# Kernel optimization log

Measured on AMD Instinct MI355X. Metric: run time of the kernel, lower is better.

## Reference

```python
import jax, jax.numpy as jnp
import numpy as np

B, S, D = 8, 4096, 64
LN_EPS = 1e-3  # keras LayerNormalization default epsilon


def setup_inputs() -> dict:
    key = jax.random.key(0)
    k1, k2 = jax.random.split(key)
    x = jax.random.normal(k1, (B, S, D), dtype=jnp.float32)
    # (D,D,D) concept tensor, scaled small like glorot-ish init
    concept_map = jax.random.normal(k2, (D, D, D), dtype=jnp.float32) * 0.02
    gamma = jnp.ones((D,), dtype=jnp.float32)
    beta = jnp.zeros((D,), dtype=jnp.float32)
    return {"x": x, "concept_map": concept_map, "gamma": gamma, "beta": beta}


def reference(x, concept_map, gamma, beta):
    b, s, d = x.shape
    # Causal Toeplitz decay matrix: T[i, j] = 1/(i-j)^2 for j < i, else 0.
    idx = jnp.arange(s)
    diff = idx[:, None] - idx[None, :]  # (S, S)
    T = jnp.where(diff > 0, 1.0 / (jnp.maximum(diff, 1).astype(x.dtype) ** 2), 0.0)
    # Weighted causal prefix sum: S_pre[b, i, c] = sum_{j<i} x[b, j, c] / (i-j)^2
    s_pre = jnp.einsum('ij,bjc->bic', T, x)
    # Bilinear form with concept tensor: out[b,i,k] = sum_{a,c} x[b,i,a] * s_pre[b,i,c] * W[k,a,c]
    outer = (x[:, :, :, None] * s_pre[:, :, None, :]).reshape(b, s, d * d)  # (B,S,D*D)
    out = outer @ concept_map.reshape(d, d * d).T  # (B,S,D)
    # Residual + LayerNorm (axis=-1, keras defaults). Dropout is identity at inference.
    r = out + x
    mu = jnp.mean(r, axis=-1, keepdims=True)
    var = jnp.mean((r - mu) ** 2, axis=-1, keepdims=True)
    y = (r - mu) / jnp.sqrt(var + LN_EPS) * gamma + beta
    return y
```

## Files before the change

### kernel.cpp

```cpp
#include <hip/hip_runtime.h>

#define S_DIM 4096
#define B_DIM 8
#define D_DIM 64
#define LN_EPS 1e-3f

typedef _Float16 half8 __attribute__((ext_vector_type(8)));
typedef float f32x4 __attribute__((ext_vector_type(4)));

__device__ __forceinline__ void async_copy16(void* lds, const void* gsrc) {
    __builtin_amdgcn_global_load_lds(
        (const __attribute__((address_space(1))) unsigned int*)gsrc,
        (__attribute__((address_space(3))) unsigned int*)lds, 16, 0, 0);
}

__global__ __launch_bounds__(256) void prep_stage1(const float* __restrict__ x,
                                                   const float* __restrict__ W,
                                                   _Float16* __restrict__ wt,
                                                   _Float16* __restrict__ s_out) {
    if (blockIdx.x < 1024) {
        int idx = blockIdx.x * 256 + threadIdx.x;
        int a = idx >> 12;
        int k = (idx >> 6) & 63;
        int c = idx & 63;
        wt[idx] = (_Float16)W[((k << 6) + a) * 64 + c];
        return;
    }
    const int lin = blockIdx.x - 1024;
    const int it = lin & 63;
    const int by = lin >> 6;
    const int i0 = it * 64;
    const int tid = threadIdx.x;
    const int w = tid >> 6, l = tid & 63, lg = l >> 4, lr = l & 15;

    __shared__ _Float16 Bs[64 * 72];

    f32x4 acc[4] = {};
    const float iRowF = (float)(i0 + w * 16 + lr);
    const int ldC = tid & 63;
    const int ldJ = (tid >> 6) * 16;

    const int jt0 = (it >= 2) ? (it - 2) : 0;
    for (int jt = jt0; jt <= it; ++jt) {
        const int j0 = jt * 64;
        __syncthreads();
        {
            const float* xp = x + ((size_t)by * S_DIM + j0 + ldJ) * D_DIM + ldC;
            half8 v0, v1;
            #pragma unroll
            for (int q = 0; q < 8; ++q) {
                v0[q] = (_Float16)xp[q * D_DIM];
                v1[q] = (_Float16)xp[(8 + q) * D_DIM];
            }
            *(half8*)&Bs[ldC * 72 + ldJ] = v0;
            *(half8*)&Bs[ldC * 72 + ldJ + 8] = v1;
        }
        __syncthreads();
        #pragma unroll
        for (int kk = 0; kk < 2; ++kk) {
            half8 af;
            #pragma unroll
            for (int bq = 0; bq < 8; ++bq) {
                int j = j0 + kk * 32 + lg * 8 + bq;
                float df = iRowF - (float)j;
                float tv = (df > 0.f) ? __builtin_amdgcn_rcpf(df * df) : 0.f;
                af[bq] = (_Float16)tv;
            }
            #pragma unroll
            for (int nt = 0; nt < 4; ++nt) {
                half8 bf = *(const half8*)&Bs[(nt * 16 + lr) * 72 + kk * 32 + lg * 8];
                acc[nt] = __builtin_amdgcn_mfma_f32_16x16x32_f16(af, bf, acc[nt], 0, 0, 0);
            }
        }
    }

    #pragma unroll
    for (int nt = 0; nt < 4; ++nt) {
        #pragma unroll
        for (int r = 0; r < 4; ++r) {
            int i = i0 + w * 16 + lg * 4 + r;
            int c = nt * 16 + lr;
            s_out[((size_t)by * S_DIM + i) * D_DIM + c] = (_Float16)acc[nt][r];
        }
    }
}

__global__ __launch_bounds__(512, 2) void stage2(const float* __restrict__ x,
                                                 const _Float16* __restrict__ s,
                                                 const _Float16* __restrict__ wt,
                                                 const float* __restrict__ gamma,
                                                 const float* __restrict__ beta,
                                                 float* __restrict__ out) {
    const int r0 = blockIdx.x * 128;
    const int tid = threadIdx.x;
    const int w = tid >> 6, l = tid & 63, lg = l >> 4, lr = l & 15;
    const int rg = w & 1;
    const int ah = w >> 1;

    __shared__ __align__(16) char smem[101376];
    _Float16* Xf = (_Float16*)smem;
    char* WbB = smem + 18432;
    float* P = (float*)smem;

    const int laneSrc = ((l >> 3) * 128) + ((((l & 7) ^ (l >> 3)) << 4));
    const char* wbase = (const char*)wt;

#define STAGE(t, buf)                                                          \
    {                                                                          \
        _Pragma("unroll")                                                      \
        for (int i_ = 0; i_ < 4; ++i_) {                                       \
            int c_ = w * 4 + i_;                                               \
            int q_ = c_ >> 3, sub_ = c_ & 7;                                   \
            const char* g_ = wbase + (size_t)(q_ * 16 + (t)) * 8192            \
                             + sub_ * 1024 + laneSrc;                          \
            char* l_ = WbB + (buf) * 32768 + q_ * 8192 + sub_ * 1024;          \
            async_copy16(l_, g_);                                              \
        }                                                                      \
    }

    STAGE(0, 0);
    STAGE(1, 1);

    {
        #pragma unroll
        for (int h = 0; h < 2; ++h) {
            int idx = h * 512 + tid;
            int row = idx >> 3, c0 = (idx & 7) * 8;
            const float* xp = x + (size_t)(r0 + row) * 64 + c0;
            half8 v;
            #pragma unroll
            for (int j = 0; j < 8; ++j) v[j] = (_Float16)xp[j];
            *(half8*)&Xf[row * 72 + c0] = v;
        }
    }

    half8 sf[4][2];
    #pragma unroll
    for (int rt = 0; rt < 4; ++rt) {
        size_t row = (size_t)(r0 + rg * 64 + rt * 16 + lr) * 64;
        sf[rt][0] = *(const half8*)&s[row + lg * 8];
        sf[rt][1] = *(const half8*)&s[row + 32 + lg * 8];
    }

    __syncthreads();

    half8 xav[4][2];
    #pragma unroll
    for (int rt = 0; rt < 4; ++rt)
        #pragma unroll
        for (int q = 0; q < 2; ++q)
            xav[rt][q] = *(const half8*)&Xf[(rg * 64 + rt * 16 + lr) * 72 + ah * 16 + q * 8];

    f32x4 acc[4][4] = {};
    const int swz0 = (lg * 16) ^ ((lr & 7) << 4);
    const int swz1 = (64 + lg * 16) ^ ((lr & 7) << 4);

    #pragma unroll
    for (int t = 0; t < 16; ++t) {
        const char* wa = WbB + (t & 1) * 32768 + ah * 8192;
        half8 af[4][2];
        #pragma unroll
        for (int rt = 0; rt < 4; ++rt) {
            _Float16 xa = xav[rt][t >> 3][t & 7];
            af[rt][0] = sf[rt][0] * xa;
            af[rt][1] = sf[rt][1] * xa;
        }
        #pragma unroll
        for (int nt = 0; nt < 4; ++nt) {
            const char* rp = wa + (nt * 16 + lr) * 128;
            half8 b0 = *(const half8*)(rp + swz0);
            half8 b1 = *(const half8*)(rp + swz1);
            #pragma unroll
            for (int rt = 0; rt < 4; ++rt) {
                acc[rt][nt] = __builtin_amdgcn_mfma_f32_16x16x32_f16(af[rt][0], b0, acc[rt][nt], 0, 0, 0);
                acc[rt][nt] = __builtin_amdgcn_mfma_f32_16x16x32_f16(af[rt][1], b1, acc[rt][nt], 0, 0, 0);
            }
        }
        __builtin_amdgcn_s_barrier();
        if (t + 2 < 16) STAGE(t + 2, t & 1);
        if (t < 14) {
            asm volatile("s_waitcnt vmcnt(4)" ::: "memory");
            __builtin_amdgcn_s_barrier();
        } else if (t == 14) {
            asm volatile("s_waitcnt vmcnt(0)" ::: "memory");
            __builtin_amdgcn_s_barrier();
        }
    }

    if (ah != 0) {
        const int ph = ah - 1;
        #pragma unroll
        for (int rt = 0; rt < 4; ++rt)
            #pragma unroll
            for (int nt = 0; nt < 4; ++nt)
                #pragma unroll
                for (int reg = 0; reg < 4; ++reg) {
                    int row_l = rg * 64 + rt * 16 + lg * 4 + reg;
                    P[ph * 8448 + row_l * 66 + nt * 16 + lr] = acc[rt][nt][reg];
                }
    }
    __syncthreads();

    if (ah == 0) {
        float gba[4], bta[4];
        #pragma unroll
        for (int nt = 0; nt < 4; ++nt) {
            gba[nt] = gamma[nt * 16 + lr];
            bta[nt] = beta[nt * 16 + lr];
        }
        #pragma unroll
        for (int rt = 0; rt < 4; ++rt) {
            float rv[4][4], sum[4], ssq[4];
            #pragma unroll
            for (int reg = 0; reg < 4; ++reg) {
                int row_l = rg * 64 + rt * 16 + lg * 4 + reg;
                size_t gr = (size_t)(r0 + row_l);
                float s_ = 0.f, q_ = 0.f;
                #pragma unroll
                for (int nt = 0; nt < 4; ++nt) {
                    int col = nt * 16 + lr;
                    float v = acc[rt][nt][reg]
                            + P[row_l * 66 + col]
                            + P[8448 + row_l * 66 + col]
                            + P[16896 + row_l * 66 + col]
                            + x[gr * 64 + col];
                    rv[nt][reg] = v;
                    s_ += v;
                    q_ += v * v;
                }
                sum[reg] = s_;
                ssq[reg] = q_;
            }
            #pragma unroll
            for (int m = 1; m < 16; m <<= 1) {
                #pragma unroll
                for (int reg = 0; reg < 4; ++reg) {
                    sum[reg] += __shfl_xor(sum[reg], m, 64);
                    ssq[reg] += __shfl_xor(ssq[reg], m, 64);
                }
            }
            #pragma unroll
            for (int reg = 0; reg < 4; ++reg) {
                float mean = sum[reg] * (1.f / 64.f);
                float var = ssq[reg] * (1.f / 64.f) - mean * mean;
                float rstd = __frsqrt_rn(var + LN_EPS);
                int gr = r0 + rg * 64 + rt * 16 + lg * 4 + reg;
                #pragma unroll
                for (int nt = 0; nt < 4; ++nt) {
                    float y = (rv[nt][reg] - mean) * rstd * gba[nt] + bta[nt];
                    out[(size_t)gr * 64 + nt * 16 + lr] = y;
                }
            }
        }
    }
#undef STAGE
}

extern "C" void kernel_launch(void* const* d_in, const int* in_sizes, int n_in,
                              void* d_out, int out_size, void* d_ws, size_t ws_size,
                              hipStream_t stream) {
    const float* x     = (const float*)d_in[0];
    const float* W     = (const float*)d_in[1];
    const float* gamma = (const float*)d_in[2];
    const float* beta  = (const float*)d_in[3];
    float* outp        = (float*)d_out;

    char* ws = (char*)d_ws;
    _Float16* s_f16 = (_Float16*)ws;
    _Float16* wt    = (_Float16*)(ws + (size_t)B_DIM * S_DIM * D_DIM * 2);

    prep_stage1<<<1024 + 512, 256, 0, stream>>>(x, W, wt, s_f16);
    stage2<<<(B_DIM * S_DIM) / 128, 512, 0, stream>>>(x, s_f16, wt, gamma, beta, outp);
}
```

Before: 33.71 us.

## Give each wave a private W slice to drop block barriers in stage2

Stage2 now uses 256-thread blocks over 64 rows. Each of the 4 waves owns a private 16 KB LDS double buffer and streams its own quarter of the `a` dimension of W, so the per-step block-wide s_barriers go away and waves synchronise only on their own vmcnt. The x tile is loaded straight from global memory into registers per wave instead of through shared LDS. All four waves now contribute partial sums to the LayerNorm epilogue through LDS. In exchange, each row block re-reads the full W per wave with no sharing, there are twice as many blocks, and total W traffic doubles.

```diff
diff --git a/kernel.cpp b/kernel.cpp
--- a/kernel.cpp
+++ b/kernel.cpp
@@ -85,71 +85,57 @@
     }
 }
 
-__global__ __launch_bounds__(512, 2) void stage2(const float* __restrict__ x,
+__global__ __launch_bounds__(256, 2) void stage2(const float* __restrict__ x,
                                                  const _Float16* __restrict__ s,
                                                  const _Float16* __restrict__ wt,
                                                  const float* __restrict__ gamma,
                                                  const float* __restrict__ beta,
                                                  float* __restrict__ out) {
-    const int r0 = blockIdx.x * 128;
+    const int r0 = blockIdx.x * 64;
     const int tid = threadIdx.x;
     const int w = tid >> 6, l = tid & 63, lg = l >> 4, lr = l & 15;
-    const int rg = w & 1;
-    const int ah = w >> 1;
-
-    __shared__ __align__(16) char smem[101376];
-    _Float16* Xf = (_Float16*)smem;
-    char* WbB = smem + 18432;
-    float* P = (float*)smem;
+
+    __shared__ __align__(16) char smem[65536];
+    char* myBuf = smem + w * 16384;
 
     const int laneSrc = ((l >> 3) * 128) + ((((l & 7) ^ (l >> 3)) << 4));
-    const char* wbase = (const char*)wt;
-
-#define STAGE(t, buf)                                                          \
+    const char* wbase = (const char*)wt + (size_t)w * 16 * 8192;
+
+#define STAGEW(t_, buf_)                                                       \
     {                                                                          \
         _Pragma("unroll")                                                      \
-        for (int i_ = 0; i_ < 4; ++i_) {                                       \
-            int c_ = w * 4 + i_;                                               \
-            int q_ = c_ >> 3, sub_ = c_ & 7;                                   \
-            const char* g_ = wbase + (size_t)(q_ * 16 + (t)) * 8192            \
-                             + sub_ * 1024 + laneSrc;                          \
-            char* l_ = WbB + (buf) * 32768 + q_ * 8192 + sub_ * 1024;          \
-            async_copy16(l_, g_);                                              \
-        }                                                                      \
-    }
-
-    STAGE(0, 0);
-    STAGE(1, 1);
-
-    {
-        #pragma unroll
-        for (int h = 0; h < 2; ++h) {
-            int idx = h * 512 + tid;
-            int row = idx >> 3, c0 = (idx & 7) * 8;
-            const float* xp = x + (size_t)(r0 + row) * 64 + c0;
-            half8 v;
-            #pragma unroll
-            for (int j = 0; j < 8; ++j) v[j] = (_Float16)xp[j];
-            *(half8*)&Xf[row * 72 + c0] = v;
-        }
+        for (int s_ = 0; s_ < 8; ++s_)                                         \
+            async_copy16(myBuf + (buf_) * 8192 + s_ * 1024,                    \
+                         wbase + (size_t)(t_) * 8192 + s_ * 1024 + laneSrc);   \
     }
 
     half8 sf[4][2];
     #pragma unroll
     for (int rt = 0; rt < 4; ++rt) {
-        size_t row = (size_t)(r0 + rg * 64 + rt * 16 + lr) * 64;
+        size_t row = (size_t)(r0 + rt * 16 + lr) * 64;
         sf[rt][0] = *(const half8*)&s[row + lg * 8];
         sf[rt][1] = *(const half8*)&s[row + 32 + lg * 8];
     }
-
-    __syncthreads();
-
     half8 xav[4][2];
     #pragma unroll
-    for (int rt = 0; rt < 4; ++rt)
-        #pragma unroll
-        for (int q = 0; q < 2; ++q)
-            xav[rt][q] = *(const half8*)&Xf[(rg * 64 + rt * 16 + lr) * 72 + ah * 16 + q * 8];
+    for (int rt = 0; rt < 4; ++rt) {
+        const float* xp = x + (size_t)(r0 + rt * 16 + lr) * 64 + w * 16;
+        half8 h0, h1;
+        #pragma unroll
+        for (int j = 0; j < 8; ++j) {
+            h0[j] = (_Float16)xp[j];
+            h1[j] = (_Float16)xp[8 + j];
+        }
+        xav[rt][0] = h0;
+        xav[rt][1] = h1;
+    }
+
+    __builtin_amdgcn_sched_barrier(0);
+    STAGEW(0, 0);
+    STAGEW(1, 1);
+    __builtin_amdgcn_sched_barrier(0);
+    asm volatile("s_waitcnt vmcnt(0)" ::: "memory");
+    __builtin_amdgcn_sched_barrier(0);
 
     f32x4 acc[4][4] = {};
     const int swz0 = (lg * 16) ^ ((lr & 7) << 4);
@@ -157,7 +143,7 @@
 
     #pragma unroll
     for (int t = 0; t < 16; ++t) {
-        const char* wa = WbB + (t & 1) * 32768 + ah * 8192;
+        const char* wa = myBuf + (t & 1) * 8192;
         half8 af[4][2];
         #pragma unroll
         for (int rt = 0; rt < 4; ++rt) {
@@ -176,84 +162,78 @@
                 acc[rt][nt] = __builtin_amdgcn_mfma_f32_16x16x32_f16(af[rt][1], b1, acc[rt][nt], 0, 0, 0);
             }
         }
-        __builtin_amdgcn_s_barrier();
-        if (t + 2 < 16) STAGE(t + 2, t & 1);
-        if (t < 14) {
-            asm volatile("s_waitcnt vmcnt(4)" ::: "memory");
-            __builtin_amdgcn_s_barrier();
+        if (t + 2 < 16) {
+            __builtin_amdgcn_sched_barrier(0);
+            STAGEW(t + 2, t & 1);
+            asm volatile("s_waitcnt vmcnt(8)" ::: "memory");
+            __builtin_amdgcn_sched_barrier(0);
         } else if (t == 14) {
             asm volatile("s_waitcnt vmcnt(0)" ::: "memory");
-            __builtin_amdgcn_s_barrier();
-        }
-    }
-
-    if (ah != 0) {
-        const int ph = ah - 1;
-        #pragma unroll
-        for (int rt = 0; rt < 4; ++rt)
-            #pragma unroll
-            for (int nt = 0; nt < 4; ++nt)
-                #pragma unroll
-                for (int reg = 0; reg < 4; ++reg) {
-                    int row_l = rg * 64 + rt * 16 + lg * 4 + reg;
-                    P[ph * 8448 + row_l * 66 + nt * 16 + lr] = acc[rt][nt][reg];
-                }
-    }
+            __builtin_amdgcn_sched_barrier(0);
+        }
+    }
+
+    float* Pw = (float*)myBuf;
+    #pragma unroll
+    for (int rt = 0; rt < 4; ++rt)
+        #pragma unroll
+        for (int nt = 0; nt < 4; ++nt)
+            #pragma unroll
+            for (int reg = 0; reg < 4; ++reg)
+                Pw[(rt * 16 + lg * 4 + reg) * 64 + nt * 16 + lr] = acc[rt][nt][reg];
     __syncthreads();
 
-    if (ah == 0) {
-        float gba[4], bta[4];
+    const float* P0 = (const float*)(smem);
+    const float* P1 = (const float*)(smem + 16384);
+    const float* P2 = (const float*)(smem + 32768);
+    const float* P3 = (const float*)(smem + 49152);
+
+    float gba[4], bta[4];
+    #pragma unroll
+    for (int nt = 0; nt < 4; ++nt) {
+        gba[nt] = gamma[nt * 16 + lr];
+        bta[nt] = beta[nt * 16 + lr];
+    }
+
+    float rv[4][4], sum[4], ssq[4];
+    #pragma unroll
+    for (int reg = 0; reg < 4; ++reg) {
+        const int row_l = w * 16 + lg * 4 + reg;
+        const float* xr = x + (size_t)(r0 + row_l) * 64;
+        float s_ = 0.f, q_ = 0.f;
         #pragma unroll
         for (int nt = 0; nt < 4; ++nt) {
-            gba[nt] = gamma[nt * 16 + lr];
-            bta[nt] = beta[nt * 16 + lr];
-        }
-        #pragma unroll
-        for (int rt = 0; rt < 4; ++rt) {
-            float rv[4][4], sum[4], ssq[4];
-            #pragma unroll
-            for (int reg = 0; reg < 4; ++reg) {
-                int row_l = rg * 64 + rt * 16 + lg * 4 + reg;
-                size_t gr = (size_t)(r0 + row_l);
-                float s_ = 0.f, q_ = 0.f;
-                #pragma unroll
-                for (int nt = 0; nt < 4; ++nt) {
-                    int col = nt * 16 + lr;
-                    float v = acc[rt][nt][reg]
-                            + P[row_l * 66 + col]
-                            + P[8448 + row_l * 66 + col]
-                            + P[16896 + row_l * 66 + col]
-                            + x[gr * 64 + col];
-                    rv[nt][reg] = v;
-                    s_ += v;
-                    q_ += v * v;
-                }
-                sum[reg] = s_;
-                ssq[reg] = q_;
-            }
-            #pragma unroll
-            for (int m = 1; m < 16; m <<= 1) {
-                #pragma unroll
-                for (int reg = 0; reg < 4; ++reg) {
-                    sum[reg] += __shfl_xor(sum[reg], m, 64);
-                    ssq[reg] += __shfl_xor(ssq[reg], m, 64);
-                }
-            }
-            #pragma unroll
-            for (int reg = 0; reg < 4; ++reg) {
-                float mean = sum[reg] * (1.f / 64.f);
-                float var = ssq[reg] * (1.f / 64.f) - mean * mean;
-                float rstd = __frsqrt_rn(var + LN_EPS);
-                int gr = r0 + rg * 64 + rt * 16 + lg * 4 + reg;
-                #pragma unroll
-                for (int nt = 0; nt < 4; ++nt) {
-                    float y = (rv[nt][reg] - mean) * rstd * gba[nt] + bta[nt];
-                    out[(size_t)gr * 64 + nt * 16 + lr] = y;
-                }
-            }
-        }
-    }
-#undef STAGE
+            const int col = nt * 16 + lr;
+            const int o = row_l * 64 + col;
+            float v = P0[o] + P1[o] + P2[o] + P3[o] + xr[col];
+            rv[nt][reg] = v;
+            s_ += v;
+            q_ += v * v;
+        }
+        sum[reg] = s_;
+        ssq[reg] = q_;
+    }
+    #pragma unroll
+    for (int m = 1; m < 16; m <<= 1) {
+        #pragma unroll
+        for (int reg = 0; reg < 4; ++reg) {
+            sum[reg] += __shfl_xor(sum[reg], m, 64);
+            ssq[reg] += __shfl_xor(ssq[reg], m, 64);
+        }
+    }
+    #pragma unroll
+    for (int reg = 0; reg < 4; ++reg) {
+        float mean = sum[reg] * (1.f / 64.f);
+        float var = ssq[reg] * (1.f / 64.f) - mean * mean;
+        float rstd = __frsqrt_rn(var + LN_EPS);
+        const int gr = r0 + w * 16 + lg * 4 + reg;
+        #pragma unroll
+        for (int nt = 0; nt < 4; ++nt) {
+            float y = (rv[nt][reg] - mean) * rstd * gba[nt] + bta[nt];
+            out[(size_t)gr * 64 + nt * 16 + lr] = y;
+        }
+    }
+#undef STAGEW
 }
 
 extern "C" void kernel_launch(void* const* d_in, const int* in_sizes, int n_in,
@@ -270,5 +250,5 @@
     _Float16* wt    = (_Float16*)(ws + (size_t)B_DIM * S_DIM * D_DIM * 2);
 
     prep_stage1<<<1024 + 512, 256, 0, stream>>>(x, W, wt, s_f16);
-    stage2<<<(B_DIM * S_DIM) / 128, 512, 0, stream>>>(x, s_f16, wt, gamma, beta, outp);
-}
+    stage2<<<(B_DIM * S_DIM) / 64, 256, 0, stream>>>(x, s_f16, wt, gamma, beta, outp);
+}
```

Measured after the change: 33.49 us. Within noise of the previous version (-0.7%).
